# Kernel optimization log

Hardware: AMD Instinct MI355X
Metric: run time of the kernel (lower is better)

## Reference

```python
import jax, jax.numpy as jnp
import numpy as np

ALPHA = 1.0
LAMBDA_CL = 1.0
EPS = 1e-08


def setup_inputs() -> dict:
    key = jax.random.key(0)
    k1, k2, k3, k4 = jax.random.split(key, 4)
    N, D_IN, D_LAT, K = 16384, 1024, 128, 256
    x = jax.random.normal(k1, (N, D_IN), dtype=jnp.float32)
    h_x = jax.random.normal(k2, (N, D_LAT), dtype=jnp.float32)
    a_x = jax.random.normal(k3, (N, D_IN), dtype=jnp.float32)
    cluster_centers = jax.random.normal(k4, (K, D_LAT), dtype=jnp.float32)
    return {"x": x, "h_x": h_x, "a_x": a_x, "cluster_centers": cluster_centers}


def _pairwise_dist(h, R):
    # Euclidean cdist via ||h||^2 + ||R||^2 - 2 h R^T (avoids [N,K,d] broadcast)
    h2 = jnp.sum(h * h, axis=1, keepdims=True)            # [N,1]
    r2 = jnp.sum(R * R, axis=1)[None, :]                   # [1,K]
    d2 = h2 + r2 - 2.0 * jnp.einsum('nd,kd->nk', h, R)     # [N,K]
    return jnp.sqrt(jnp.maximum(d2, 0.0))


def reference(x, h_x, a_x, cluster_centers):
    # Reconstruction MSE
    loss_reconstr = jnp.mean((x - a_x) ** 2)
    # Alpha-smoothed soft assignments (note +EPS in denominator, as in original)
    dist = _pairwise_dist(h_x, cluster_centers)            # [N,K]
    e = jnp.exp(-ALPHA * dist)                             # [N,K]
    soft_assignments = e / (jnp.sum(e, axis=1, keepdims=True) + EPS)
    # Weighted centers and clustering MSE
    weighted_centers = jnp.einsum('nk,kd->nd', soft_assignments, cluster_centers)
    loss_clustering = jnp.mean((h_x - weighted_centers) ** 2)
    return loss_reconstr + LAMBDA_CL * loss_clustering
```

## Files before the change

### kernel.cpp

```cpp
#include <hip/hip_runtime.h>
#include <math.h>

#define N_ROWS 16384
#define D_INP  1024
#define D_LAT  128
#define KC     256
#define EPS_F  1e-8f

typedef _Float16 half8v __attribute__((ext_vector_type(8)));
typedef __attribute__((ext_vector_type(4))) float floatx4;
typedef __attribute__((ext_vector_type(4))) float f4v;

__device__ __forceinline__ unsigned short f2h(float f) {
    _Float16 h = (_Float16)f;
    unsigned short u;
    __builtin_memcpy(&u, &h, 2);
    return u;
}
__device__ __forceinline__ float h2f(unsigned short u) {
    _Float16 h;
    __builtin_memcpy(&h, &u, 2);
    return (float)h;
}

__global__ __launch_bounds__(256) void prep_kernel(const float* __restrict__ R,
        unsigned short* __restrict__ Rf16, unsigned short* __restrict__ Rt16,
        float* __restrict__ r2) {
    const int t = threadIdx.x;
    const int kc = blockIdx.x * 2 + (t >> 7);
    const int d = t & 127;
    const float v = R[kc * D_LAT + d];
    Rf16[kc * D_LAT + d] = f2h(v);
    Rt16[d * KC + kc] = f2h(v);
    float sq = v * v;
    for (int off = 32; off > 0; off >>= 1) sq += __shfl_down(sq, off);
    __shared__ float s4[4];
    if ((t & 63) == 0) s4[t >> 6] = sq;
    __syncthreads();
    if (t == 0)   r2[kc] = s4[0] + s4[1];
    if (t == 128) r2[kc] = s4[2] + s4[3];
}

__global__ __launch_bounds__(512) void fused_kernel(
        const float* __restrict__ x, const float* __restrict__ a,
        const float* __restrict__ h,
        const unsigned short* __restrict__ Rf16,
        const unsigned short* __restrict__ Rt16,
        const float* __restrict__ r2w,
        float* __restrict__ pr, float* __restrict__ pc) {
    __shared__ unsigned short sh16[64 * 136];
    __shared__ unsigned short eL[64 * 264];
    __shared__ float sumsL[64][16];
    __shared__ float h2L[64];
    __shared__ float invL[64];
    __shared__ float swL[8];

    const int bid = blockIdx.x;
    const int tid = threadIdx.x;
    const int wv = tid >> 6, lane = tid & 63;

    if (bid % 5 != 0) {
        const int rid = bid - 1 - bid / 5;
        const int gid = rid * 512 + tid;
        const f4v* x4 = (const f4v*)x;
        const f4v* a4 = (const f4v*)a;
        f4v xv[8], av[8];
#pragma unroll
        for (int it = 0; it < 8; ++it) {
            const int i = gid + it * (512 * 1024);
            xv[it] = __builtin_nontemporal_load(x4 + i);
            av[it] = __builtin_nontemporal_load(a4 + i);
        }
        float a0 = 0.f, a1 = 0.f, a2 = 0.f, a3 = 0.f;
#pragma unroll
        for (int it = 0; it < 8; ++it) {
            const float d0 = xv[it].x - av[it].x, d1 = xv[it].y - av[it].y;
            const float d2 = xv[it].z - av[it].z, d3 = xv[it].w - av[it].w;
            a0 = fmaf(d0, d0, a0);
            a1 = fmaf(d1, d1, a1);
            a2 = fmaf(d2, d2, a2);
            a3 = fmaf(d3, d3, a3);
        }
        float acc = (a0 + a1) + (a2 + a3);
        for (int off = 32; off > 0; off >>= 1) acc += __shfl_down(acc, off);
        if (lane == 0) swL[wv] = acc;
        __syncthreads();
        if (tid == 0) {
            float t = 0.f;
#pragma unroll
            for (int w = 0; w < 8; ++w) t += swL[w];
            pr[rid] = t;
        }
        return;
    }

    const int cid = bid / 5;
    const int rbase = cid * 64;
    const int g = lane >> 4, c = lane & 15;

    {
        const int r = tid >> 3, c8 = tid & 7;
        const float* hrow = h + (size_t)(rbase + r) * D_LAT;
        float s = 0.f;
#pragma unroll
        for (int q = 0; q < 4; ++q) {
            const int c4 = c8 + q * 8;
            const f4v v = __builtin_nontemporal_load((const f4v*)(hrow + c4 * 4));
            sh16[r * 136 + c4 * 4 + 0] = f2h(v.x);
            sh16[r * 136 + c4 * 4 + 1] = f2h(v.y);
            sh16[r * 136 + c4 * 4 + 2] = f2h(v.z);
            sh16[r * 136 + c4 * 4 + 3] = f2h(v.w);
            s = fmaf(v.x, v.x, s);
            s = fmaf(v.y, v.y, s);
            s = fmaf(v.z, v.z, s);
            s = fmaf(v.w, v.w, s);
        }
        s += __shfl_xor(s, 1);
        s += __shfl_xor(s, 2);
        s += __shfl_xor(s, 4);
        if ((tid & 7) == 0) h2L[r] = s;
    }
    __syncthreads();

    {
        half8v bA[2][4];
#pragma unroll
        for (int tt = 0; tt < 2; ++tt) {
            const int kc = (wv * 2 + tt) * 16 + c;
#pragma unroll
            for (int ks = 0; ks < 4; ++ks)
                bA[tt][ks] = *(const half8v*)(Rf16 + (size_t)kc * D_LAT + ks * 32 + g * 8);
        }
        const float r2v[2] = {r2w[wv * 32 + c], r2w[wv * 32 + 16 + c]};
#pragma unroll
        for (int rt = 0; rt < 4; ++rt) {
            half8v aH[4];
#pragma unroll
            for (int ks = 0; ks < 4; ++ks)
                aH[ks] = *(const half8v*)&sh16[(rt * 16 + c) * 136 + ks * 32 + g * 8];
            float h2a[4];
#pragma unroll
            for (int i = 0; i < 4; ++i) h2a[i] = h2L[rt * 16 + 4 * g + i];
#pragma unroll
            for (int tt = 0; tt < 2; ++tt) {
                floatx4 acc = {0.f, 0.f, 0.f, 0.f};
#pragma unroll
                for (int ks = 0; ks < 4; ++ks)
                    acc = __builtin_amdgcn_mfma_f32_16x16x32_f16(aH[ks], bA[tt][ks], acc, 0, 0, 0);
                const int kc = (wv * 2 + tt) * 16 + c;
#pragma unroll
                for (int i = 0; i < 4; ++i) {
                    const float d2 = h2a[i] + r2v[tt] - 2.0f * acc[i];
                    const float e = __expf(-sqrtf(fmaxf(d2, 0.f)));
                    eL[(rt * 16 + 4 * g + i) * 264 + kc] = f2h(e);
                    float v = e;
                    v += __shfl_xor(v, 1);
                    v += __shfl_xor(v, 2);
                    v += __shfl_xor(v, 4);
                    v += __shfl_xor(v, 8);
                    if (c == 0) sumsL[rt * 16 + 4 * g + i][wv * 2 + tt] = v;
                }
            }
        }
    }
    __syncthreads();
    if (tid < 64) {
        float t = 0.f;
#pragma unroll
        for (int j = 0; j < 16; ++j) t += sumsL[tid][j];
        invL[tid] = 1.0f / (t + EPS_F);
    }
    __syncthreads();

    {
        const int dcol = wv * 16 + c;
        half8v bB[8];
#pragma unroll
        for (int ks = 0; ks < 8; ++ks)
            bB[ks] = *(const half8v*)(Rt16 + (size_t)dcol * KC + ks * 32 + g * 8);
        float lp = 0.f;
#pragma unroll
        for (int rt = 0; rt < 4; ++rt) {
            floatx4 acc = {0.f, 0.f, 0.f, 0.f};
#pragma unroll
            for (int ks = 0; ks < 8; ++ks) {
                const half8v ae = *(const half8v*)&eL[(rt * 16 + c) * 264 + ks * 32 + g * 8];
                acc = __builtin_amdgcn_mfma_f32_16x16x32_f16(ae, bB[ks], acc, 0, 0, 0);
            }
#pragma unroll
            for (int i = 0; i < 4; ++i) {
                const int row = rt * 16 + 4 * g + i;
                const float wc = acc[i] * invL[row];
                const float hv = h2f(sh16[row * 136 + dcol]);
                const float df = hv - wc;
                lp = fmaf(df, df, lp);
            }
        }
        for (int off = 32; off > 0; off >>= 1) lp += __shfl_down(lp, off);
        if (lane == 0) swL[wv] = lp;
    }
    __syncthreads();
    if (tid == 0) {
        float t = 0.f;
#pragma unroll
        for (int w = 0; w < 8; ++w) t += swL[w];
        pc[cid] = t;
    }
}

__global__ __launch_bounds__(256) void finalize_kernel(const float* __restrict__ pr,
                                                       const float* __restrict__ pc,
                                                       float* __restrict__ out) {
    const int tid = threadIdx.x;
    float a = 0.f, b = 0.f;
    for (int i = tid; i < 1024; i += 256) a += pr[i];
    if (tid < 256) b = pc[tid];
    float v = a * (1.0f / ((float)N_ROWS * (float)D_INP)) +
              b * (1.0f / ((float)N_ROWS * (float)D_LAT));
    for (int off = 32; off > 0; off >>= 1) v += __shfl_down(v, off);
    __shared__ float sw[4];
    if ((tid & 63) == 0) sw[tid >> 6] = v;
    __syncthreads();
    if (tid == 0) out[0] = sw[0] + sw[1] + sw[2] + sw[3];
}

extern "C" void kernel_launch(void* const* d_in, const int* in_sizes, int n_in,
                              void* d_out, int out_size, void* d_ws, size_t ws_size,
                              hipStream_t stream) {
    const float* x = (const float*)d_in[0];
    const float* h = (const float*)d_in[1];
    const float* a = (const float*)d_in[2];
    const float* R = (const float*)d_in[3];
    float* out = (float*)d_out;
    char* wsb = (char*)d_ws;
    float* pr = (float*)(wsb + 0);
    float* pc = (float*)(wsb + 8192);
    float* r2 = (float*)(wsb + 12288);
    unsigned short* Rf16 = (unsigned short*)(wsb + 16384);
    unsigned short* Rt16 = (unsigned short*)(wsb + 16384 + 65536);

    prep_kernel<<<128, 256, 0, stream>>>(R, Rf16, Rt16, r2);
    fused_kernel<<<1280, 512, 0, stream>>>(x, a, h, Rf16, Rt16, r2, pr, pc);
    finalize_kernel<<<1, 256, 0, stream>>>(pr, pc, out);
}
```

Measured before the change: 44.61 us.

## Merge prep, fused and finalize kernels into one with last-block reduction

Removes the separate prep kernel by converting cluster centers to fp16 and computing their squared norms inside each clustering block. The finalize kernel is replaced by an atomic-counter last-block reduction, with a memset resetting the counter. This cuts two kernel launches and their inter-kernel gaps. In exchange, each clustering block redoes the center conversion and reads R transposed with strided scalar loads in the second GEMM.

```diff
diff --git a/kernel.cpp b/kernel.cpp
--- a/kernel.cpp
+++ b/kernel.cpp
@@ -6,6 +6,7 @@
 #define D_LAT  128
 #define KC     256
 #define EPS_F  1e-8f
+#define NBLK   1280
 
 typedef _Float16 half8v __attribute__((ext_vector_type(8)));
 typedef __attribute__((ext_vector_type(4))) float floatx4;
@@ -23,37 +24,19 @@
     return (float)h;
 }
 
-__global__ __launch_bounds__(256) void prep_kernel(const float* __restrict__ R,
-        unsigned short* __restrict__ Rf16, unsigned short* __restrict__ Rt16,
-        float* __restrict__ r2) {
-    const int t = threadIdx.x;
-    const int kc = blockIdx.x * 2 + (t >> 7);
-    const int d = t & 127;
-    const float v = R[kc * D_LAT + d];
-    Rf16[kc * D_LAT + d] = f2h(v);
-    Rt16[d * KC + kc] = f2h(v);
-    float sq = v * v;
-    for (int off = 32; off > 0; off >>= 1) sq += __shfl_down(sq, off);
-    __shared__ float s4[4];
-    if ((t & 63) == 0) s4[t >> 6] = sq;
-    __syncthreads();
-    if (t == 0)   r2[kc] = s4[0] + s4[1];
-    if (t == 128) r2[kc] = s4[2] + s4[3];
-}
-
-__global__ __launch_bounds__(512) void fused_kernel(
+__global__ __launch_bounds__(512) void mono_kernel(
         const float* __restrict__ x, const float* __restrict__ a,
-        const float* __restrict__ h,
-        const unsigned short* __restrict__ Rf16,
-        const unsigned short* __restrict__ Rt16,
-        const float* __restrict__ r2w,
-        float* __restrict__ pr, float* __restrict__ pc) {
+        const float* __restrict__ h, const float* __restrict__ R,
+        float* __restrict__ pr, float* __restrict__ pc,
+        unsigned* __restrict__ counter, float* __restrict__ out) {
     __shared__ unsigned short sh16[64 * 136];
     __shared__ unsigned short eL[64 * 264];
     __shared__ float sumsL[64][16];
+    __shared__ float r2L[KC];
     __shared__ float h2L[64];
     __shared__ float invL[64];
     __shared__ float swL[8];
+    __shared__ int lastFlag;
 
     const int bid = blockIdx.x;
     const int tid = threadIdx.x;
@@ -91,137 +74,168 @@
             for (int w = 0; w < 8; ++w) t += swL[w];
             pr[rid] = t;
         }
-        return;
+    } else {
+        const int cid = bid / 5;
+        const int rbase = cid * 64;
+        const int g = lane >> 4, c = lane & 15;
+
+        {
+            const int r = tid >> 3, c8 = tid & 7;
+            const float* hrow = h + (size_t)(rbase + r) * D_LAT;
+            float s = 0.f;
+#pragma unroll
+            for (int q = 0; q < 4; ++q) {
+                const int c4 = c8 + q * 8;
+                const f4v v = __builtin_nontemporal_load((const f4v*)(hrow + c4 * 4));
+                sh16[r * 136 + c4 * 4 + 0] = f2h(v.x);
+                sh16[r * 136 + c4 * 4 + 1] = f2h(v.y);
+                sh16[r * 136 + c4 * 4 + 2] = f2h(v.z);
+                sh16[r * 136 + c4 * 4 + 3] = f2h(v.w);
+                s = fmaf(v.x, v.x, s);
+                s = fmaf(v.y, v.y, s);
+                s = fmaf(v.z, v.z, s);
+                s = fmaf(v.w, v.w, s);
+            }
+            s += __shfl_xor(s, 1);
+            s += __shfl_xor(s, 2);
+            s += __shfl_xor(s, 4);
+            if ((tid & 7) == 0) h2L[r] = s;
+        }
+
+        half8v bA[2][4];
+#pragma unroll
+        for (int tt = 0; tt < 2; ++tt) {
+            const int kc = (wv * 2 + tt) * 16 + c;
+            float s = 0.f;
+#pragma unroll
+            for (int ks = 0; ks < 4; ++ks) {
+                const float* rp = R + (size_t)kc * D_LAT + ks * 32 + g * 8;
+                const f4v p0 = *(const f4v*)rp;
+                const f4v p1 = *(const f4v*)(rp + 4);
+                half8v b;
+                b[0] = (_Float16)p0.x; b[1] = (_Float16)p0.y;
+                b[2] = (_Float16)p0.z; b[3] = (_Float16)p0.w;
+                b[4] = (_Float16)p1.x; b[5] = (_Float16)p1.y;
+                b[6] = (_Float16)p1.z; b[7] = (_Float16)p1.w;
+                bA[tt][ks] = b;
+                s = fmaf(p0.x, p0.x, s); s = fmaf(p0.y, p0.y, s);
+                s = fmaf(p0.z, p0.z, s); s = fmaf(p0.w, p0.w, s);
+                s = fmaf(p1.x, p1.x, s); s = fmaf(p1.y, p1.y, s);
+                s = fmaf(p1.z, p1.z, s); s = fmaf(p1.w, p1.w, s);
+            }
+            s += __shfl_xor(s, 16);
+            s += __shfl_xor(s, 32);
+            if (g == 0) r2L[kc] = s;
+        }
+        __syncthreads();
+
+        {
+            const float r2v[2] = {r2L[wv * 32 + c], r2L[wv * 32 + 16 + c]};
+#pragma unroll
+            for (int rt = 0; rt < 4; ++rt) {
+                half8v aH[4];
+#pragma unroll
+                for (int ks = 0; ks < 4; ++ks)
+                    aH[ks] = *(const half8v*)&sh16[(rt * 16 + c) * 136 + ks * 32 + g * 8];
+                float h2a[4];
+#pragma unroll
+                for (int i = 0; i < 4; ++i) h2a[i] = h2L[rt * 16 + 4 * g + i];
+#pragma unroll
+                for (int tt = 0; tt < 2; ++tt) {
+                    floatx4 acc = {0.f, 0.f, 0.f, 0.f};
+#pragma unroll
+                    for (int ks = 0; ks < 4; ++ks)
+                        acc = __builtin_amdgcn_mfma_f32_16x16x32_f16(aH[ks], bA[tt][ks], acc, 0, 0, 0);
+                    const int kc = (wv * 2 + tt) * 16 + c;
+#pragma unroll
+                    for (int i = 0; i < 4; ++i) {
+                        const float d2 = h2a[i] + r2v[tt] - 2.0f * acc[i];
+                        const float e = __expf(-sqrtf(fmaxf(d2, 0.f)));
+                        eL[(rt * 16 + 4 * g + i) * 264 + kc] = f2h(e);
+                        float v = e;
+                        v += __shfl_xor(v, 1);
+                        v += __shfl_xor(v, 2);
+                        v += __shfl_xor(v, 4);
+                        v += __shfl_xor(v, 8);
+                        if (c == 0) sumsL[rt * 16 + 4 * g + i][wv * 2 + tt] = v;
+                    }
+                }
+            }
+        }
+        __syncthreads();
+        if (tid < 64) {
+            float t = 0.f;
+#pragma unroll
+            for (int j = 0; j < 16; ++j) t += sumsL[tid][j];
+            invL[tid] = 1.0f / (t + EPS_F);
+        }
+        __syncthreads();
+
+        {
+            const int dcol = wv * 16 + c;
+            half8v bB[8];
+#pragma unroll
+            for (int ks = 0; ks < 8; ++ks) {
+                const int kb = ks * 32 + g * 8;
+                half8v b;
+#pragma unroll
+                for (int j = 0; j < 8; ++j)
+                    b[j] = (_Float16)R[(size_t)(kb + j) * D_LAT + dcol];
+                bB[ks] = b;
+            }
+            float lp = 0.f;
+#pragma unroll
+            for (int rt = 0; rt < 4; ++rt) {
+                floatx4 acc = {0.f, 0.f, 0.f, 0.f};
+#pragma unroll
+                for (int ks = 0; ks < 8; ++ks) {
+                    const half8v ae = *(const half8v*)&eL[(rt * 16 + c) * 264 + ks * 32 + g * 8];
+                    acc = __builtin_amdgcn_mfma_f32_16x16x32_f16(ae, bB[ks], acc, 0, 0, 0);
+                }
+#pragma unroll
+                for (int i = 0; i < 4; ++i) {
+                    const int row = rt * 16 + 4 * g + i;
+                    const float wc = acc[i] * invL[row];
+                    const float hv = h2f(sh16[row * 136 + dcol]);
+                    const float df = hv - wc;
+                    lp = fmaf(df, df, lp);
+                }
+            }
+            for (int off = 32; off > 0; off >>= 1) lp += __shfl_down(lp, off);
+            if (lane == 0) swL[wv] = lp;
+        }
+        __syncthreads();
+        if (tid == 0) {
+            float t = 0.f;
+#pragma unroll
+            for (int w = 0; w < 8; ++w) t += swL[w];
+            pc[cid] = t;
+        }
     }
 
-    const int cid = bid / 5;
-    const int rbase = cid * 64;
-    const int g = lane >> 4, c = lane & 15;
-
-    {
-        const int r = tid >> 3, c8 = tid & 7;
-        const float* hrow = h + (size_t)(rbase + r) * D_LAT;
-        float s = 0.f;
-#pragma unroll
-        for (int q = 0; q < 4; ++q) {
-            const int c4 = c8 + q * 8;
-            const f4v v = __builtin_nontemporal_load((const f4v*)(hrow + c4 * 4));
-            sh16[r * 136 + c4 * 4 + 0] = f2h(v.x);
-            sh16[r * 136 + c4 * 4 + 1] = f2h(v.y);
-            sh16[r * 136 + c4 * 4 + 2] = f2h(v.z);
-            sh16[r * 136 + c4 * 4 + 3] = f2h(v.w);
-            s = fmaf(v.x, v.x, s);
-            s = fmaf(v.y, v.y, s);
-            s = fmaf(v.z, v.z, s);
-            s = fmaf(v.w, v.w, s);
-        }
-        s += __shfl_xor(s, 1);
-        s += __shfl_xor(s, 2);
-        s += __shfl_xor(s, 4);
-        if ((tid & 7) == 0) h2L[r] = s;
+    if (tid == 0) {
+        __threadfence();
+        lastFlag = (atomicAdd(counter, 1u) == NBLK - 1);
     }
     __syncthreads();
-
-    {
-        half8v bA[2][4];
-#pragma unroll
-        for (int tt = 0; tt < 2; ++tt) {
-            const int kc = (wv * 2 + tt) * 16 + c;
-#pragma unroll
-            for (int ks = 0; ks < 4; ++ks)
-                bA[tt][ks] = *(const half8v*)(Rf16 + (size_t)kc * D_LAT + ks * 32 + g * 8);
-        }
-        const float r2v[2] = {r2w[wv * 32 + c], r2w[wv * 32 + 16 + c]};
-#pragma unroll
-        for (int rt = 0; rt < 4; ++rt) {
-            half8v aH[4];
-#pragma unroll
-            for (int ks = 0; ks < 4; ++ks)
-                aH[ks] = *(const half8v*)&sh16[(rt * 16 + c) * 136 + ks * 32 + g * 8];
-            float h2a[4];
-#pragma unroll
-            for (int i = 0; i < 4; ++i) h2a[i] = h2L[rt * 16 + 4 * g + i];
-#pragma unroll
-            for (int tt = 0; tt < 2; ++tt) {
-                floatx4 acc = {0.f, 0.f, 0.f, 0.f};
-#pragma unroll
-                for (int ks = 0; ks < 4; ++ks)
-                    acc = __builtin_amdgcn_mfma_f32_16x16x32_f16(aH[ks], bA[tt][ks], acc, 0, 0, 0);
-                const int kc = (wv * 2 + tt) * 16 + c;
-#pragma unroll
-                for (int i = 0; i < 4; ++i) {
-                    const float d2 = h2a[i] + r2v[tt] - 2.0f * acc[i];
-                    const float e = __expf(-sqrtf(fmaxf(d2, 0.f)));
-                    eL[(rt * 16 + 4 * g + i) * 264 + kc] = f2h(e);
-                    float v = e;
-                    v += __shfl_xor(v, 1);
-                    v += __shfl_xor(v, 2);
-                    v += __shfl_xor(v, 4);
-                    v += __shfl_xor(v, 8);
-                    if (c == 0) sumsL[rt * 16 + 4 * g + i][wv * 2 + tt] = v;
-                }
-            }
+    if (lastFlag) {
+        __threadfence();
+        float aa = 0.f, bb = 0.f;
+        for (int i = tid; i < 1024; i += 512) aa += pr[i];
+        if (tid < 256) bb = pc[tid];
+        float v = aa * (1.0f / ((float)N_ROWS * (float)D_INP)) +
+                  bb * (1.0f / ((float)N_ROWS * (float)D_LAT));
+        for (int off = 32; off > 0; off >>= 1) v += __shfl_down(v, off);
+        __syncthreads();
+        if (lane == 0) swL[wv] = v;
+        __syncthreads();
+        if (tid == 0) {
+            float t = 0.f;
+#pragma unroll
+            for (int w = 0; w < 8; ++w) t += swL[w];
+            out[0] = t;
         }
     }
-    __syncthreads();
-    if (tid < 64) {
-        float t = 0.f;
-#pragma unroll
-        for (int j = 0; j < 16; ++j) t += sumsL[tid][j];
-        invL[tid] = 1.0f / (t + EPS_F);
-    }
-    __syncthreads();
-
-    {
-        const int dcol = wv * 16 + c;
-        half8v bB[8];
-#pragma unroll
-        for (int ks = 0; ks < 8; ++ks)
-            bB[ks] = *(const half8v*)(Rt16 + (size_t)dcol * KC + ks * 32 + g * 8);
-        float lp = 0.f;
-#pragma unroll
-        for (int rt = 0; rt < 4; ++rt) {
-            floatx4 acc = {0.f, 0.f, 0.f, 0.f};
-#pragma unroll
-            for (int ks = 0; ks < 8; ++ks) {
-                const half8v ae = *(const half8v*)&eL[(rt * 16 + c) * 264 + ks * 32 + g * 8];
-                acc = __builtin_amdgcn_mfma_f32_16x16x32_f16(ae, bB[ks], acc, 0, 0, 0);
-            }
-#pragma unroll
-            for (int i = 0; i < 4; ++i) {
-                const int row = rt * 16 + 4 * g + i;
-                const float wc = acc[i] * invL[row];
-                const float hv = h2f(sh16[row * 136 + dcol]);
-                const float df = hv - wc;
-                lp = fmaf(df, df, lp);
-            }
-        }
-        for (int off = 32; off > 0; off >>= 1) lp += __shfl_down(lp, off);
-        if (lane == 0) swL[wv] = lp;
-    }
-    __syncthreads();
-    if (tid == 0) {
-        float t = 0.f;
-#pragma unroll
-        for (int w = 0; w < 8; ++w) t += swL[w];
-        pc[cid] = t;
-    }
-}
-
-__global__ __launch_bounds__(256) void finalize_kernel(const float* __restrict__ pr,
-                                                       const float* __restrict__ pc,
-                                                       float* __restrict__ out) {
-    const int tid = threadIdx.x;
-    float a = 0.f, b = 0.f;
-    for (int i = tid; i < 1024; i += 256) a += pr[i];
-    if (tid < 256) b = pc[tid];
-    float v = a * (1.0f / ((float)N_ROWS * (float)D_INP)) +
-              b * (1.0f / ((float)N_ROWS * (float)D_LAT));
-    for (int off = 32; off > 0; off >>= 1) v += __shfl_down(v, off);
-    __shared__ float sw[4];
-    if ((tid & 63) == 0) sw[tid >> 6] = v;
-    __syncthreads();
-    if (tid == 0) out[0] = sw[0] + sw[1] + sw[2] + sw[3];
 }
 
 extern "C" void kernel_launch(void* const* d_in, const int* in_sizes, int n_in,
@@ -234,12 +248,9 @@
     float* out = (float*)d_out;
     char* wsb = (char*)d_ws;
     float* pr = (float*)(wsb + 0);
-    float* pc = (float*)(wsb + 8192);
-    float* r2 = (float*)(wsb + 12288);
-    unsigned short* Rf16 = (unsigned short*)(wsb + 16384);
-    unsigned short* Rt16 = (unsigned short*)(wsb + 16384 + 65536);
-
-    prep_kernel<<<128, 256, 0, stream>>>(R, Rf16, Rt16, r2);
-    fused_kernel<<<1280, 512, 0, stream>>>(x, a, h, Rf16, Rt16, r2, pr, pc);
-    finalize_kernel<<<1, 256, 0, stream>>>(pr, pc, out);
-}
+    float* pc = (float*)(wsb + 4096);
+    unsigned* counter = (unsigned*)(wsb + 8192);
+
+    hipMemsetAsync(counter, 0, 4, stream);
+    mono_kernel<<<NBLK, 512, 0, stream>>>(x, a, h, R, pr, pc, counter, out);
+}
```

Result: slower. 102.0 us (+128.6%).
